# Optimization experiments

Hardware: AMD Instinct MI355X
Metric: run time of the kernel (lower is better)

Reference implementation:

```python
import jax, jax.numpy as jnp
import numpy as np

B, S, HID = 1, 2048, 2048
NH, NKV, HD = 32, 8, 64
INTER = 8192
EPS = 1e-6


def rmsnorm(x, w, eps=EPS):
    xf = x.astype(jnp.float32)
    inv = jax.lax.rsqrt(jnp.mean(xf * xf, axis=-1, keepdims=True) + eps)
    return (xf * inv * w).astype(x.dtype)


def rope(x, sin_t, cos_t):
    # x: [B, S, H, D]; sin/cos: [S, D//2]
    sin = sin_t[None, :, None, :]
    cos = cos_t[None, :, None, :]
    d2 = x.shape[-1] // 2
    x0, x1 = x[..., :d2], x[..., d2:]
    return jnp.concatenate((x0 * cos - x1 * sin, x0 * sin + x1 * cos), axis=-1)


def setup_inputs() -> dict:
    key = jax.random.key(0)
    ks = jax.random.split(key, 12)
    hidden_states = jax.random.normal(ks[0], (B, S, HID), dtype=jnp.float32)
    # realistic RoPE tables
    inv_freq = 1.0 / (10000.0 ** (np.arange(0, HD // 2, dtype=np.float32) * 2.0 / HD))
    ang = np.arange(S, dtype=np.float32)[:, None] * inv_freq[None, :]
    sin_table = jnp.asarray(np.sin(ang))
    cos_table = jnp.asarray(np.cos(ang))
    s = 0.02
    return {
        "hidden_states": hidden_states,
        "sin_table": sin_table,
        "cos_table": cos_table,
        "ln1_w": jnp.ones((HID,), jnp.float32),
        "ln2_w": jnp.ones((HID,), jnp.float32),
        "wq": jax.random.normal(ks[1], (HID, NH * HD), jnp.float32) * s,
        "wk": jax.random.normal(ks[2], (HID, NKV * HD), jnp.float32) * s,
        "wv": jax.random.normal(ks[3], (HID, NKV * HD), jnp.float32) * s,
        "wo": jax.random.normal(ks[4], (NH * HD, HID), jnp.float32) * s,
        "w_gate": jax.random.normal(ks[5], (HID, INTER), jnp.float32) * s,
        "w_up": jax.random.normal(ks[6], (HID, INTER), jnp.float32) * s,
        "w_down": jax.random.normal(ks[7], (INTER, HID), jnp.float32) * s,
    }


def attention(x, sin_t, cos_t, wq, wk, wv, wo):
    b, s, _ = x.shape
    q = (x @ wq).reshape(b, s, NH, HD)
    k = (x @ wk).reshape(b, s, NKV, HD)
    v = (x @ wv).reshape(b, s, NKV, HD).transpose(0, 2, 1, 3)  # [B,Hk,S,D]
    q = rope(q, sin_t, cos_t).transpose(0, 2, 1, 3)  # [B,Hq,S,D]
    k = rope(k, sin_t, cos_t).transpose(0, 2, 1, 3)  # [B,Hk,S,D]
    g = NH // NKV
    k = jnp.repeat(k, g, axis=1)
    v = jnp.repeat(v, g, axis=1)
    scale = 1.0 / np.sqrt(HD)
    scores = jnp.einsum("bhqd,bhkd->bhqk", q, k) * scale
    mask = jnp.tril(jnp.ones((s, s), dtype=bool))
    scores = jnp.where(mask, scores, -jnp.inf)
    probs = jax.nn.softmax(scores, axis=-1)
    out = jnp.einsum("bhqk,bhkd->bhqd", probs, v)
    out = out.transpose(0, 2, 1, 3).reshape(b, s, NH * HD)
    return out @ wo


def reference(hidden_states, sin_table, cos_table, ln1_w, ln2_w, wq, wk, wv, wo, w_gate, w_up, w_down):
    x = hidden_states
    x = x + attention(rmsnorm(x, ln1_w), sin_table, cos_table, wq, wk, wv, wo)
    h = rmsnorm(x, ln2_w)
    x = x + (jax.nn.silu(h @ w_gate) * (h @ w_up)) @ w_down
    return x
```

## Files before the change

kernel.cpp:

```cpp
#include <hip/hip_runtime.h>
#include <hip/hip_bf16.h>

typedef float f32x4 __attribute__((ext_vector_type(4)));
typedef unsigned int u32x4 __attribute__((ext_vector_type(4)));
typedef unsigned int u32x2 __attribute__((ext_vector_type(2)));
typedef _Float16 f16x4 __attribute__((ext_vector_type(4)));
typedef unsigned short u16;

#define S_LEN 2048
#define HID 2048
#define NHEAD 32
#define NKVH 8
#define HDIM 64

__device__ __forceinline__ unsigned short f2bf_bits(float f) {
    unsigned int u = __builtin_bit_cast(unsigned int, f);
    unsigned int r = u + 0x7fffu + ((u >> 16) & 1u);
    return (unsigned short)(r >> 16);
}
__device__ __forceinline__ float bf2f(unsigned short b) {
    unsigned int u = ((unsigned int)b) << 16;
    return __builtin_bit_cast(float, u);
}
__device__ __forceinline__ unsigned cvt_pk_bf16(float lo, float hi) {
    unsigned d;
    asm("v_cvt_pk_bf16_f32 %0, %1, %2" : "=v"(d) : "v"(lo), "v"(hi));
    return d;
}

__device__ __forceinline__ f32x4 mfma_bf16(u32x4 a, u32x4 b, f32x4 c) {
    asm("v_mfma_f32_16x16x32_bf16 %0, %1, %2, %0" : "+v"(c) : "v"(a), "v"(b));
    return c;
}

__device__ __forceinline__ void gload_lds16(const void* g, void* l) {
    __builtin_amdgcn_global_load_lds(
        (const __attribute__((address_space(1))) void*)g,
        (__attribute__((address_space(3))) void*)l, 16, 0, 0);
}

__global__ __launch_bounds__(256)
void rmsnorm_k(const float* __restrict__ x, const float* __restrict__ wgt,
               unsigned short* __restrict__ out)
{
    int row = blockIdx.x;
    int t = threadIdx.x;
    const float* xr = x + (size_t)row * HID;
    f32x4 a = *(const f32x4*)(xr + t * 8);
    f32x4 b = *(const f32x4*)(xr + t * 8 + 4);
    float s = 0.f;
#pragma unroll
    for (int i = 0; i < 4; ++i) s += a[i] * a[i] + b[i] * b[i];
#pragma unroll
    for (int off = 32; off > 0; off >>= 1) s += __shfl_down(s, off);
    __shared__ float red[4];
    if ((t & 63) == 0) red[t >> 6] = s;
    __syncthreads();
    float tot = red[0] + red[1] + red[2] + red[3];
    float inv = rsqrtf(tot * (1.0f / (float)HID) + 1e-6f);
    f32x4 wa = *(const f32x4*)(wgt + t * 8);
    f32x4 wb = *(const f32x4*)(wgt + t * 8 + 4);
    unsigned int pk[4];
#pragma unroll
    for (int i = 0; i < 2; ++i) {
        pk[i]     = (unsigned)f2bf_bits(a[2*i] * inv * wa[2*i]) |
                    ((unsigned)f2bf_bits(a[2*i+1] * inv * wa[2*i+1]) << 16);
        pk[i + 2] = (unsigned)f2bf_bits(b[2*i] * inv * wb[2*i]) |
                    ((unsigned)f2bf_bits(b[2*i+1] * inv * wb[2*i+1]) << 16);
    }
    u32x4 ov; ov[0] = pk[0]; ov[1] = pk[1]; ov[2] = pk[2]; ov[3] = pk[3];
    *(u32x4*)(out + (size_t)row * HID + t * 8) = ov;
}

__global__ __launch_bounds__(256)
void transpose_cvt(const float* __restrict__ in, unsigned short* __restrict__ out,
                   int K, int N)
{
    __shared__ unsigned short tile[64 * 65];
    int kb = blockIdx.y * 64, nb = blockIdx.x * 64;
    int t = threadIdx.x;
    int r = t >> 2, c0 = (t & 3) * 16;
    const float* src = in + (size_t)(kb + r) * N + nb + c0;
#pragma unroll
    for (int j = 0; j < 4; ++j) {
        f32x4 v = *(const f32x4*)(src + j * 4);
#pragma unroll
        for (int i = 0; i < 4; ++i)
            tile[r * 65 + c0 + j * 4 + i] = f2bf_bits(v[i]);
    }
    __syncthreads();
    unsigned short e[16];
#pragma unroll
    for (int j = 0; j < 16; ++j) e[j] = tile[(c0 + j) * 65 + r];
    u32x4 o0, o1;
#pragma unroll
    for (int j = 0; j < 4; ++j) {
        o0[j] = (unsigned)e[2*j] | ((unsigned)e[2*j+1] << 16);
        o1[j] = (unsigned)e[8 + 2*j] | ((unsigned)e[8 + 2*j+1] << 16);
    }
    unsigned short* dst = out + (size_t)(nb + r) * K + kb + c0;
    *(u32x4*)(dst) = o0;
    *(u32x4*)(dst + 8) = o1;
}

__global__ __launch_bounds__(256)
void rope_k(unsigned short* __restrict__ qkv, const float* __restrict__ sin_t,
            const float* __restrict__ cos_t)
{
    int s = blockIdx.x;
    for (int it = threadIdx.x; it < (NHEAD + NKVH) * 32; it += 256) {
        int slot = it >> 5;
        int d = it & 31;
        int col = (slot < NHEAD) ? slot * 64 + d : HID + (slot - NHEAD) * 64 + d;
        unsigned short* p = qkv + (size_t)s * 3072 + col;
        float x0 = bf2f(p[0]);
        float x1 = bf2f(p[32]);
        float c = cos_t[s * 32 + d];
        float sn = sin_t[s * 32 + d];
        p[0]  = f2bf_bits(x0 * c - x1 * sn);
        p[32] = f2bf_bits(x0 * sn + x1 * c);
    }
}

__global__ __launch_bounds__(256)
void transpose_v(const unsigned short* __restrict__ qkv, unsigned short* __restrict__ vT)
{
    __shared__ unsigned short tile[64][80];
    int kb = blockIdx.x * 64, kvh = blockIdx.y;
    int t = threadIdx.x;
    int r = t >> 2, c0 = (t & 3) * 16;
    const unsigned short* src = qkv + (size_t)(kb + r) * 3072 + 2560 + kvh * 64 + c0;
    u32x4 v0 = *(const u32x4*)(src);
    u32x4 v1 = *(const u32x4*)(src + 8);
    *(u32x4*)&tile[r][c0] = v0;
    *(u32x4*)&tile[r][c0 + 8] = v1;
    __syncthreads();
    int d = t >> 2, k0 = (t & 3) * 16;
    unsigned short e[16];
#pragma unroll
    for (int j = 0; j < 16; ++j) e[j] = tile[k0 + j][d];
    u32x4 o0, o1;
#pragma unroll
    for (int j = 0; j < 4; ++j) {
        o0[j] = (unsigned)e[2*j] | ((unsigned)e[2*j+1] << 16);
        o1[j] = (unsigned)e[8 + 2*j] | ((unsigned)e[8 + 2*j+1] << 16);
    }
    int s0 = ((k0 >> 3) ^ (d & 7)) & 7;
    int s1 = (((k0 >> 3) + 1) ^ (d & 7)) & 7;
    unsigned short* dst = vT + ((size_t)kvh * 64 + d) * 2048 + kb;
    *(u32x4*)(dst + s0 * 8) = o0;
    *(u32x4*)(dst + s1 * 8) = o1;
}

template <int EPI>
__global__ __launch_bounds__(256)
void gemm_bt(const unsigned short* __restrict__ A,
             const unsigned short* __restrict__ Bt,
             void* __restrict__ outp, const void* __restrict__ auxp,
             int M, int N, int Kc, int lda)
{
    __shared__ unsigned short As[2][128 * 32];
    __shared__ unsigned short Bs[2][128 * 32];
    int t = threadIdx.x, w = t >> 6, l = t & 63;
    int rb = blockIdx.y, cb = blockIdx.x, zb = blockIdx.z;
    int wr = w >> 1, wc = w & 1;
    int l4 = l >> 4, l15 = l & 15;
    int arow = l >> 2, acol = (l & 3) * 8;
    f32x4 acc[4][4] = {};
    const unsigned short* Ag = A + (size_t)rb * 128 * lda + (size_t)zb * Kc
                                 + (size_t)(w * 16 + arow) * lda + acol;
    const unsigned short* Bg = Bt + (size_t)cb * 128 * lda + (size_t)zb * Kc
                                 + (size_t)(w * 16 + arow) * lda + acol;
    int nk = Kc >> 5;

#define STAGE(buf, kt)                                                          \
    {                                                                           \
        const unsigned short* Agk = Ag + (size_t)(kt) * 32;                     \
        const unsigned short* Bgk = Bg + (size_t)(kt) * 32;                     \
        gload_lds16(Agk, &As[buf][w * 512]);                                    \
        gload_lds16(Agk + (size_t)64 * lda, &As[buf][(4 + w) * 512]);           \
        gload_lds16(Bgk, &Bs[buf][w * 512]);                                    \
        gload_lds16(Bgk + (size_t)64 * lda, &Bs[buf][(4 + w) * 512]);           \
    }

    STAGE(0, 0);
    __syncthreads();
    int cur = 0;
    for (int kt = 0; kt < nk; ++kt) {
        if (kt + 1 < nk) STAGE(cur ^ 1, kt + 1);
        u32x4 af[4], bfr[4];
#pragma unroll
        for (int i = 0; i < 4; ++i)
            af[i] = *(const u32x4*)(&As[cur][(wr * 64 + i * 16 + l15) * 32 + l4 * 8]);
#pragma unroll
        for (int n = 0; n < 4; ++n)
            bfr[n] = *(const u32x4*)(&Bs[cur][(wc * 64 + n * 16 + l15) * 32 + l4 * 8]);
#pragma unroll
        for (int i = 0; i < 4; ++i)
#pragma unroll
            for (int n = 0; n < 4; ++n)
                acc[i][n] = mfma_bf16(af[i], bfr[n], acc[i][n]);
        __syncthreads();
        cur ^= 1;
    }
#undef STAGE

    int row0 = rb * 128 + wr * 64 + l4 * 4;
    int col0 = cb * 128 + wc * 64 + l15;
#pragma unroll
    for (int i = 0; i < 4; ++i) {
#pragma unroll
        for (int n = 0; n < 4; ++n) {
#pragma unroll
            for (int r = 0; r < 4; ++r) {
                int row = row0 + i * 16 + r;
                int col = col0 + n * 16;
                size_t idx = (size_t)row * N + col;
                float v = acc[i][n][r];
                if (EPI == 0) {
                    ((unsigned short*)outp)[idx] = f2bf_bits(v);
                } else if (EPI == 3) {
                    ((float*)outp)[idx] = v + ((const float*)auxp)[idx];
                } else {
                    ((_Float16*)outp)[(size_t)zb * M * N + idx] = (_Float16)v;
                }
            }
        }
    }
}

template <int KK, int QUAD>
__device__ __forceinline__ void phase8(u16* lds, int cur, f32x4 (&acc)[8][4],
                                       u32x4 (&bfv)[4],
                                       int aoff, int boff,
                                       const u16* Asrc, const u16* Bsrc,
                                       int lda, int kt_stage,
                                       int dst0, int dst1)
{
    const u16* ah = lds + (cur * 4 + KK * 2) * 8192 + aoff + QUAD * 2048;
    u32x4 af[4];
#pragma unroll
    for (int mi = 0; mi < 4; ++mi) af[mi] = *(const u32x4*)(ah + mi * 512);
    if (QUAD == 0) {
        const u16* bh = lds + (cur * 4 + KK * 2 + 1) * 8192 + boff;
#pragma unroll
        for (int ni = 0; ni < 4; ++ni) bfv[ni] = *(const u32x4*)(bh + ni * 512);
    }
    {
        const u16* src = (QUAD ? Bsrc : Asrc) + (size_t)kt_stage * 64 + (KK == 0 ? 32 : 0);
        int dbuf = (KK == 0) ? (cur ^ 1) : cur;
        int slot = (KK == 0) ? (2 + QUAD) : QUAD;
        u16* d = lds + (dbuf * 4 + slot) * 8192;
        gload_lds16(src, d + dst0);
        gload_lds16(src + (size_t)128 * lda, d + dst1);
    }
    __builtin_amdgcn_s_barrier();
    asm volatile("s_waitcnt lgkmcnt(0)" ::: "memory");
    __builtin_amdgcn_sched_barrier(0);
    __builtin_amdgcn_s_setprio(1);
#pragma unroll
    for (int mi = 0; mi < 4; ++mi)
#pragma unroll
        for (int ni = 0; ni < 4; ++ni)
            acc[QUAD * 4 + mi][ni] = mfma_bf16(af[mi], bfv[ni], acc[QUAD * 4 + mi][ni]);
    __builtin_amdgcn_s_setprio(0);
    if (QUAD == 1) asm volatile("s_waitcnt vmcnt(8)" ::: "memory");
    __builtin_amdgcn_s_barrier();
}

template <int EPI>
__global__ __launch_bounds__(512, 2)
void gemm8p(const u16* __restrict__ A, const u16* __restrict__ Bt,
            void* __restrict__ outp, const void* __restrict__ auxp,
            int M, int N, int Kc, int lda)
{
    extern __shared__ u16 lds[];
    const int tid = threadIdx.x;
    const int w = tid >> 6, l = tid & 63;
    const int wm = w >> 2, wn = w & 3;
    const int l4 = l >> 4, l15 = l & 15;
    const int zb = blockIdx.y;

    int wg = blockIdx.x, nwg = gridDim.x;
    int swzb = ((nwg & 7) == 0) ? ((wg & 7) * (nwg >> 3) + (wg >> 3)) : wg;
    int rbs = M >> 8;
    int rb = swzb % rbs, cb = swzb / rbs;

    const int sw = ((tid & 3) ^ ((tid >> 3) & 3)) * 8;
    const int srow = tid >> 2;
    const u16* Asrc = A + (size_t)(rb * 256 + srow) * lda + (size_t)zb * Kc + sw;
    const u16* Bsrc = Bt + (size_t)(cb * 256 + srow) * lda + (size_t)zb * Kc + sw;
    const int dst0 = tid * 8, dst1 = (512 + tid) * 8;

    const int rswz = (l15 >> 1) & 3;
    const int aoff = (wm * 128 + l15) * 32 + (l4 ^ rswz) * 8;
    const int boff = (wn * 64 + l15) * 32 + (l4 ^ rswz) * 8;

    f32x4 acc[8][4] = {};
    u32x4 bfv[4];
    const int NT = Kc >> 6;

    {
#pragma unroll
        for (int h = 0; h < 2; ++h) {
            const u16* sA = Asrc + h * 32;
            const u16* sB = Bsrc + h * 32;
            gload_lds16(sA, lds + (h * 2) * 8192 + dst0);
            gload_lds16(sA + (size_t)128 * lda, lds + (h * 2) * 8192 + dst1);
            gload_lds16(sB, lds + (h * 2 + 1) * 8192 + dst0);
            gload_lds16(sB + (size_t)128 * lda, lds + (h * 2 + 1) * 8192 + dst1);
        }
        int t1 = (NT > 1) ? 1 : 0;
        const u16* sA = Asrc + (size_t)t1 * 64;
        const u16* sB = Bsrc + (size_t)t1 * 64;
        gload_lds16(sA, lds + (4 + 0) * 8192 + dst0);
        gload_lds16(sA + (size_t)128 * lda, lds + (4 + 0) * 8192 + dst1);
        gload_lds16(sB, lds + (4 + 1) * 8192 + dst0);
        gload_lds16(sB + (size_t)128 * lda, lds + (4 + 1) * 8192 + dst1);
    }
    asm volatile("s_waitcnt vmcnt(8)" ::: "memory");
    __builtin_amdgcn_s_barrier();

    for (int t = 0; t < NT; ++t) {
        int cur = t & 1;
        int k1 = (t + 1 < NT) ? t + 1 : 0;
        int k2 = (t + 2 < NT) ? t + 2 : 0;
        phase8<0, 0>(lds, cur, acc, bfv, aoff, boff, Asrc, Bsrc, lda, k1, dst0, dst1);
        phase8<0, 1>(lds, cur, acc, bfv, aoff, boff, Asrc, Bsrc, lda, k1, dst0, dst1);
        phase8<1, 0>(lds, cur, acc, bfv, aoff, boff, Asrc, Bsrc, lda, k2, dst0, dst1);
        phase8<1, 1>(lds, cur, acc, bfv, aoff, boff, Asrc, Bsrc, lda, k2, dst0, dst1);
    }
    asm volatile("s_waitcnt vmcnt(0)" ::: "memory");

    int row0 = rb * 256 + wm * 128 + l4 * 4;
    int col0 = cb * 256 + wn * 64 + l15;
#pragma unroll
    for (int mi = 0; mi < 8; ++mi) {
#pragma unroll
        for (int ni = 0; ni < 4; ++ni) {
#pragma unroll
            for (int r = 0; r < 4; ++r) {
                int row = row0 + mi * 16 + r;
                int col = col0 + ni * 16;
                size_t idx = (size_t)row * N + col;
                float v = acc[mi][ni][r];
                if (EPI == 1) {
                    float sv = v / (1.0f + __expf(-v));
                    ((unsigned short*)outp)[idx] = f2bf_bits(sv);
                } else if (EPI == 2) {
                    float gv = bf2f(((const unsigned short*)auxp)[idx]);
                    ((unsigned short*)outp)[idx] = f2bf_bits(v * gv);
                } else {
                    ((_Float16*)outp)[(size_t)zb * M * N + idx] = (_Float16)v;
                }
            }
        }
    }
}

__global__ __launch_bounds__(256)
void reduce_add4(float* __restrict__ out, const _Float16* __restrict__ p, int n)
{
    int i = (blockIdx.x * 256 + threadIdx.x) * 4;
    f32x4 a = *(const f32x4*)(out + i);
#pragma unroll
    for (int z = 0; z < 4; ++z) {
        f16x4 h = *(const f16x4*)(p + (size_t)z * n + i);
#pragma unroll
        for (int j = 0; j < 4; ++j) a[j] += (float)h[j];
    }
    *(f32x4*)(out + i) = a;
}

__global__ __launch_bounds__(256)
void reduce_res2(float* __restrict__ out, const float* __restrict__ x,
                 const _Float16* __restrict__ p, int n)
{
    int i = (blockIdx.x * 256 + threadIdx.x) * 4;
    f32x4 a = *(const f32x4*)(x + i);
#pragma unroll
    for (int z = 0; z < 2; ++z) {
        f16x4 h = *(const f16x4*)(p + (size_t)z * n + i);
#pragma unroll
        for (int j = 0; j < 4; ++j) a[j] += (float)h[j];
    }
    *(f32x4*)(out + i) = a;
}

__global__ __launch_bounds__(256)
void attn_fwd(const unsigned short* __restrict__ qkv,
              const unsigned short* __restrict__ vT,
              unsigned short* __restrict__ out)
{
    int p = blockIdx.x, h = blockIdx.y, kvh = h >> 2;
    int t = threadIdx.x, w = t >> 6, l = t & 63;
    int l4 = l >> 4, l15 = l & 15;
    __shared__ unsigned short Ks[2][64 * 64];
    __shared__ unsigned short Vs[2][64 * 64];

    const unsigned short* Kg = qkv + HID + kvh * 64;
    const unsigned short* Vg = vT + (size_t)kvh * 64 * 2048;

    int ch0 = w * 2, ch1 = w * 2 + 1;
    int rsub = l >> 3;
    int ksw = ((l & 7) ^ (rsub & 7)) * 8;
    int vcol = (l & 7) * 8;
    int sw0 = (l4 ^ (l15 & 7)) * 8;
    int sw1 = ((l4 | 4) ^ (l15 & 7)) * 8;
    int srcA = ((l >> 4) & 1) * 32 + l15;
    int srcB = srcA + 16;
    bool hi32 = (l & 32) != 0;

#define STAGE_KV(buf, kt)                                                         \
    {                                                                             \
        gload_lds16(Kg + (size_t)((kt) * 64 + ch0 * 8 + rsub) * 3072 + ksw,       \
                    &Ks[buf][ch0 * 512]);                                         \
        gload_lds16(Kg + (size_t)((kt) * 64 + ch1 * 8 + rsub) * 3072 + ksw,       \
                    &Ks[buf][ch1 * 512]);                                         \
        gload_lds16(Vg + (size_t)(ch0 * 8 + rsub) * 2048 + (kt) * 64 + vcol,      \
                    &Vs[buf][ch0 * 512]);                                         \
        gload_lds16(Vg + (size_t)(ch1 * 8 + rsub) * 2048 + (kt) * 64 + vcol,      \
                    &Vs[buf][ch1 * 512]);                                         \
    }

    const float SC2 = 0.18033688f;
    const float THR = 44.36f;
    const float BIG = -3.0e38f;

    for (int half = 0; half < 2; ++half) {
        int qb = half ? (31 - p) : p;
        int qrow0 = qb * 64 + w * 16;
        STAGE_KV(0, 0);
        const unsigned short* qg = qkv + (size_t)(qrow0 + l15) * 3072 + h * 64 + l4 * 8;
        u32x4 aq0 = *(const u32x4*)(qg);
        u32x4 aq1 = *(const u32x4*)(qg + 32);
        f32x4 o[4] = {};
        float m = BIG, ls = 0.f;
        __syncthreads();
        int cur = 0;
        for (int kt = 0; kt <= qb; ++kt) {
            if (kt < qb) STAGE_KV(cur ^ 1, kt + 1);
            f32x4 sc[4];
#pragma unroll
            for (int n = 0; n < 4; ++n) {
                const unsigned short* kb_ = &Ks[cur][(n * 16 + l15) * 64];
                u32x4 b0 = *(const u32x4*)(kb_ + sw0);
                u32x4 b1 = *(const u32x4*)(kb_ + sw1);
                f32x4 z = {};
                z = mfma_bf16(b0, aq0, z);
                z = mfma_bf16(b1, aq1, z);
                sc[n] = z;
            }
            if (kt == qb) {
                int qloc = w * 16 + l15;
#pragma unroll
                for (int n = 0; n < 4; ++n)
#pragma unroll
                    for (int r = 0; r < 4; ++r)
                        if (n * 16 + l4 * 4 + r > qloc) sc[n][r] = BIG;
            }
            float rmax = BIG;
#pragma unroll
            for (int n = 0; n < 4; ++n)
#pragma unroll
                for (int r = 0; r < 4; ++r) rmax = fmaxf(rmax, sc[n][r]);
            rmax = fmaxf(rmax, __shfl_xor(rmax, 16));
            rmax = fmaxf(rmax, __shfl_xor(rmax, 32));
            if (__ballot(rmax - m > THR)) {
                float mn = fmaxf(m, rmax);
                float al = __builtin_exp2f((m - mn) * SC2);
                m = mn;
                ls *= al;
#pragma unroll
                for (int nd = 0; nd < 4; ++nd)
#pragma unroll
                    for (int r = 0; r < 4; ++r) o[nd][r] *= al;
            }
            float ms = m * SC2, rs = 0.f;
#pragma unroll
            for (int n = 0; n < 4; ++n)
#pragma unroll
                for (int r = 0; r < 4; ++r) {
                    float pe = __builtin_exp2f(__builtin_fmaf(sc[n][r], SC2, -ms));
                    sc[n][r] = pe;
                    rs += pe;
                }
            rs += __shfl_xor(rs, 16);
            rs += __shfl_xor(rs, 32);
            ls += rs;
            unsigned pk0[2], pk1[2], pk2[2], pk3[2];
#pragma unroll
            for (int rr = 0; rr < 2; ++rr) {
                pk0[rr] = cvt_pk_bf16(sc[0][2*rr], sc[0][2*rr+1]);
                pk1[rr] = cvt_pk_bf16(sc[1][2*rr], sc[1][2*rr+1]);
                pk2[rr] = cvt_pk_bf16(sc[2][2*rr], sc[2][2*rr+1]);
                pk3[rr] = cvt_pk_bf16(sc[3][2*rr], sc[3][2*rr+1]);
            }
            u32x4 W1, W2;
            {
                unsigned a0, a1;
                a0 = __shfl(pk0[0], srcA); a1 = __shfl(pk1[0], srcA); W1[0] = hi32 ? a1 : a0;
                a0 = __shfl(pk0[1], srcA); a1 = __shfl(pk1[1], srcA); W1[1] = hi32 ? a1 : a0;
                a0 = __shfl(pk0[0], srcB); a1 = __shfl(pk1[0], srcB); W1[2] = hi32 ? a1 : a0;
                a0 = __shfl(pk0[1], srcB); a1 = __shfl(pk1[1], srcB); W1[3] = hi32 ? a1 : a0;
                a0 = __shfl(pk2[0], srcA); a1 = __shfl(pk3[0], srcA); W2[0] = hi32 ? a1 : a0;
                a0 = __shfl(pk2[1], srcA); a1 = __shfl(pk3[1], srcA); W2[1] = hi32 ? a1 : a0;
                a0 = __shfl(pk2[0], srcB); a1 = __shfl(pk3[0], srcB); W2[2] = hi32 ? a1 : a0;
                a0 = __shfl(pk2[1], srcB); a1 = __shfl(pk3[1], srcB); W2[3] = hi32 ? a1 : a0;
            }
#pragma unroll
            for (int nd = 0; nd < 4; ++nd) {
                const unsigned short* vb = &Vs[cur][(nd * 16 + l15) * 64];
                u32x4 bv0 = *(const u32x4*)(vb + sw0);
                u32x4 bv1 = *(const u32x4*)(vb + sw1);
                o[nd] = mfma_bf16(bv0, W1, o[nd]);
                o[nd] = mfma_bf16(bv1, W2, o[nd]);
            }
            __syncthreads();
            cur ^= 1;
        }
#undef STAGE_KV
        float linv = 1.0f / ls;
        unsigned short* orow = out + (size_t)(qrow0 + l15) * HID + h * 64 + l4 * 4;
#pragma unroll
        for (int nd = 0; nd < 4; ++nd) {
            u32x2 wv;
            wv[0] = cvt_pk_bf16(o[nd][0] * linv, o[nd][1] * linv);
            wv[1] = cvt_pk_bf16(o[nd][2] * linv, o[nd][3] * linv);
            *(u32x2*)(orow + nd * 16) = wv;
        }
    }
}

extern "C" void kernel_launch(void* const* d_in, const int* in_sizes, int n_in,
                              void* d_out, int out_size, void* d_ws, size_t ws_size,
                              hipStream_t stream)
{
    const float* x     = (const float*)d_in[0];
    const float* sin_t = (const float*)d_in[1];
    const float* cos_t = (const float*)d_in[2];
    const float* ln1w  = (const float*)d_in[3];
    const float* ln2w  = (const float*)d_in[4];
    const float* wq    = (const float*)d_in[5];
    const float* wk    = (const float*)d_in[6];
    const float* wv    = (const float*)d_in[7];
    const float* wo    = (const float*)d_in[8];
    const float* wg    = (const float*)d_in[9];
    const float* wu    = (const float*)d_in[10];
    const float* wd    = (const float*)d_in[11];
    float* out = (float*)d_out;

    char* ws = (char*)d_ws;
    if (ws_size < 113246208u) return;
    unsigned short* wT   = (unsigned short*)(ws);
    unsigned short* xn   = (unsigned short*)(ws + 33554432u);
    unsigned short* qkv  = (unsigned short*)(ws + 41943040u);
    unsigned short* attn = (unsigned short*)(ws + 54525952u);
    unsigned short* vT   = (unsigned short*)(ws + 62914560u);
    _Float16*       part = (_Float16*)(ws + 33554432u);
    unsigned short* g    = (unsigned short*)(ws + 79691776u);
    _Float16*       opart = (_Float16*)(ws + 79691776u);

    hipFuncSetAttribute(reinterpret_cast<const void*>(&gemm8p<1>),
                        hipFuncAttributeMaxDynamicSharedMemorySize, 131072);
    hipFuncSetAttribute(reinterpret_cast<const void*>(&gemm8p<2>),
                        hipFuncAttributeMaxDynamicSharedMemorySize, 131072);
    hipFuncSetAttribute(reinterpret_cast<const void*>(&gemm8p<5>),
                        hipFuncAttributeMaxDynamicSharedMemorySize, 131072);

    rmsnorm_k<<<S_LEN, 256, 0, stream>>>(x, ln1w, xn);

    transpose_cvt<<<dim3(32, 32), 256, 0, stream>>>(wq, wT, 2048, 2048);
    transpose_cvt<<<dim3(8, 32), 256, 0, stream>>>(wk, wT + (size_t)2048 * 2048, 2048, 512);
    transpose_cvt<<<dim3(8, 32), 256, 0, stream>>>(wv, wT + (size_t)2560 * 2048, 2048, 512);

    gemm_bt<0><<<dim3(24, 16, 1), 256, 0, stream>>>(xn, wT, qkv, nullptr, 2048, 3072, 2048, 2048);

    rope_k<<<S_LEN, 256, 0, stream>>>(qkv, sin_t, cos_t);
    transpose_v<<<dim3(32, 8), 256, 0, stream>>>(qkv, vT);

    attn_fwd<<<dim3(16, 32), 256, 0, stream>>>(qkv, vT, attn);

    transpose_cvt<<<dim3(32, 32), 256, 0, stream>>>(wo, wT, 2048, 2048);
    gemm_bt<5><<<dim3(16, 16, 2), 256, 0, stream>>>(attn, wT, opart, nullptr, 2048, 2048, 1024, 2048);
    reduce_res2<<<4096, 256, 0, stream>>>(out, x, opart, 4194304);

    rmsnorm_k<<<S_LEN, 256, 0, stream>>>(out, ln2w, xn);

    transpose_cvt<<<dim3(128, 32), 256, 0, stream>>>(wg, wT, 2048, 8192);
    gemm8p<1><<<dim3(256, 1), 512, 131072, stream>>>(xn, wT, g, nullptr, 2048, 8192, 2048, 2048);

    transpose_cvt<<<dim3(128, 32), 256, 0, stream>>>(wu, wT, 2048, 8192);
    gemm8p<2><<<dim3(256, 1), 512, 131072, stream>>>(xn, wT, g, g, 2048, 8192, 2048, 2048);

    transpose_cvt<<<dim3(32, 128), 256, 0, stream>>>(wd, wT, 8192, 2048);
    gemm8p<5><<<dim3(64, 4), 512, 131072, stream>>>(g, wT, part, nullptr, 2048, 2048, 2048, 8192);

    reduce_add4<<<4096, 256, 0, stream>>>(out, part, 4194304);
}
```

Before: 450.0 us.

## Fuse gate and up projections into one GEMM with SiLU-multiply epilogue

Adds a gemm8p_gu kernel that loads both the gate and up weight tiles for the same 128-column block and computes both accumulators in one pass. It applies silu(gate)*up in the epilogue and writes bf16 once, instead of writing g and re-reading it in a second GEMM. This removes one full read of the activations and a 32 MB intermediate round trip. The output projection also moves from gemm_bt with split-K 2 to gemm8p with split-K 4, and the residual reduce now sums four partials. The cost is a larger per-block working set, 32 accumulator tiles per wave, and a workspace layout reshuffled so the wu transpose lands where qkv/attn previously lived.

```diff
diff --git a/kernel.cpp b/kernel.cpp
--- a/kernel.cpp
+++ b/kernel.cpp
@@ -358,6 +358,134 @@
     }
 }
 
+template <int KK, int QUAD>
+__device__ __forceinline__ void phase8gu(u16* lds, int cur, f32x4 (&acc)[8][4],
+                                         u32x4 (&bfv)[4],
+                                         int aoff, int boffg, int boffu,
+                                         const u16* Asrc, const u16* Bg, const u16* Bu,
+                                         int lda, int kt_stage,
+                                         int dst0, int dst1)
+{
+    const u16* ah = lds + (cur * 4 + KK * 2) * 8192 + aoff + QUAD * 2048;
+    u32x4 af[4];
+#pragma unroll
+    for (int mi = 0; mi < 4; ++mi) af[mi] = *(const u32x4*)(ah + mi * 512);
+    if (QUAD == 0) {
+        const u16* bh = lds + (cur * 4 + KK * 2 + 1) * 8192;
+#pragma unroll
+        for (int ni = 0; ni < 2; ++ni) {
+            bfv[ni]     = *(const u32x4*)(bh + boffg + ni * 512);
+            bfv[ni + 2] = *(const u32x4*)(bh + boffu + ni * 512);
+        }
+    }
+    {
+        int koff = (size_t)0 + (KK == 0 ? 32 : 0);
+        int dbuf = (KK == 0) ? (cur ^ 1) : cur;
+        int slot = (KK == 0) ? (2 + QUAD) : QUAD;
+        u16* d = lds + (dbuf * 4 + slot) * 8192;
+        if (QUAD == 0) {
+            const u16* src = Asrc + (size_t)kt_stage * 64 + koff;
+            gload_lds16(src, d + dst0);
+            gload_lds16(src + (size_t)128 * lda, d + dst1);
+        } else {
+            gload_lds16(Bg + (size_t)kt_stage * 64 + koff, d + dst0);
+            gload_lds16(Bu + (size_t)kt_stage * 64 + koff, d + dst1);
+        }
+    }
+    __builtin_amdgcn_s_barrier();
+    asm volatile("s_waitcnt lgkmcnt(0)" ::: "memory");
+    __builtin_amdgcn_sched_barrier(0);
+    __builtin_amdgcn_s_setprio(1);
+#pragma unroll
+    for (int mi = 0; mi < 4; ++mi)
+#pragma unroll
+        for (int ni = 0; ni < 4; ++ni)
+            acc[QUAD * 4 + mi][ni] = mfma_bf16(af[mi], bfv[ni], acc[QUAD * 4 + mi][ni]);
+    __builtin_amdgcn_s_setprio(0);
+    if (QUAD == 1) asm volatile("s_waitcnt vmcnt(8)" ::: "memory");
+    __builtin_amdgcn_s_barrier();
+}
+
+__global__ __launch_bounds__(512, 2)
+void gemm8p_gu(const u16* __restrict__ A, const u16* __restrict__ WgT,
+               const u16* __restrict__ WuT, unsigned short* __restrict__ outp,
+               int M, int Nfull, int K)
+{
+    extern __shared__ u16 lds[];
+    const int tid = threadIdx.x;
+    const int w = tid >> 6, l = tid & 63;
+    const int wm = w >> 2, wn = w & 3;
+    const int l4 = l >> 4, l15 = l & 15;
+
+    int wg = blockIdx.x, nwg = gridDim.x;
+    int swzb = ((nwg & 7) == 0) ? ((wg & 7) * (nwg >> 3) + (wg >> 3)) : wg;
+    int rbs = M >> 8;
+    int rb = swzb % rbs, cb = swzb / rbs;
+
+    const int sw = ((tid & 3) ^ ((tid >> 3) & 3)) * 8;
+    const int srow = tid >> 2;
+    const u16* Asrc = A + (size_t)(rb * 256 + srow) * K + sw;
+    const u16* Bg = WgT + (size_t)(cb * 128 + srow) * K + sw;
+    const u16* Bu = WuT + (size_t)(cb * 128 + srow) * K + sw;
+    const int dst0 = tid * 8, dst1 = (512 + tid) * 8;
+
+    const int rswz = (l15 >> 1) & 3;
+    const int aoff  = (wm * 128 + l15) * 32 + (l4 ^ rswz) * 8;
+    const int boffg = (wn * 32 + l15) * 32 + (l4 ^ rswz) * 8;
+    const int boffu = (128 + wn * 32 + l15) * 32 + (l4 ^ rswz) * 8;
+
+    f32x4 acc[8][4] = {};
+    u32x4 bfv[4];
+    const int NT = K >> 6;
+
+    {
+#pragma unroll
+        for (int h = 0; h < 2; ++h) {
+            const u16* sA = Asrc + h * 32;
+            gload_lds16(sA, lds + (h * 2) * 8192 + dst0);
+            gload_lds16(sA + (size_t)128 * K, lds + (h * 2) * 8192 + dst1);
+            gload_lds16(Bg + h * 32, lds + (h * 2 + 1) * 8192 + dst0);
+            gload_lds16(Bu + h * 32, lds + (h * 2 + 1) * 8192 + dst1);
+        }
+        const u16* sA = Asrc + 64;
+        gload_lds16(sA, lds + (4 + 0) * 8192 + dst0);
+        gload_lds16(sA + (size_t)128 * K, lds + (4 + 0) * 8192 + dst1);
+        gload_lds16(Bg + 64, lds + (4 + 1) * 8192 + dst0);
+        gload_lds16(Bu + 64, lds + (4 + 1) * 8192 + dst1);
+    }
+    asm volatile("s_waitcnt vmcnt(8)" ::: "memory");
+    __builtin_amdgcn_s_barrier();
+
+    for (int t = 0; t < NT; ++t) {
+        int cur = t & 1;
+        int k1 = (t + 1 < NT) ? t + 1 : 0;
+        int k2 = (t + 2 < NT) ? t + 2 : 0;
+        phase8gu<0, 0>(lds, cur, acc, bfv, aoff, boffg, boffu, Asrc, Bg, Bu, K, k1, dst0, dst1);
+        phase8gu<0, 1>(lds, cur, acc, bfv, aoff, boffg, boffu, Asrc, Bg, Bu, K, k1, dst0, dst1);
+        phase8gu<1, 0>(lds, cur, acc, bfv, aoff, boffg, boffu, Asrc, Bg, Bu, K, k2, dst0, dst1);
+        phase8gu<1, 1>(lds, cur, acc, bfv, aoff, boffg, boffu, Asrc, Bg, Bu, K, k2, dst0, dst1);
+    }
+    asm volatile("s_waitcnt vmcnt(0)" ::: "memory");
+
+    int row0 = rb * 256 + wm * 128 + l4 * 4;
+    int col0 = cb * 128 + wn * 32 + l15;
+#pragma unroll
+    for (int mi = 0; mi < 8; ++mi) {
+#pragma unroll
+        for (int ni = 0; ni < 2; ++ni) {
+#pragma unroll
+            for (int r = 0; r < 4; ++r) {
+                int row = row0 + mi * 16 + r;
+                int col = col0 + ni * 16;
+                float gv = acc[mi][ni][r];
+                float uv = acc[mi][ni + 2][r];
+                float sv = gv / (1.0f + __expf(-gv)) * uv;
+                outp[(size_t)row * Nfull + col] = f2bf_bits(sv);
+            }
+        }
+    }
+}
+
 __global__ __launch_bounds__(256)
 void reduce_add4(float* __restrict__ out, const _Float16* __restrict__ p, int n)
 {
@@ -373,13 +501,13 @@
 }
 
 __global__ __launch_bounds__(256)
-void reduce_res2(float* __restrict__ out, const float* __restrict__ x,
+void reduce_res4(float* __restrict__ out, const float* __restrict__ x,
                  const _Float16* __restrict__ p, int n)
 {
     int i = (blockIdx.x * 256 + threadIdx.x) * 4;
     f32x4 a = *(const f32x4*)(x + i);
 #pragma unroll
-    for (int z = 0; z < 2; ++z) {
+    for (int z = 0; z < 4; ++z) {
         f16x4 h = *(const f16x4*)(p + (size_t)z * n + i);
 #pragma unroll
         for (int j = 0; j < 4; ++j) a[j] += (float)h[j];
@@ -552,20 +680,19 @@
 
     char* ws = (char*)d_ws;
     if (ws_size < 113246208u) return;
-    unsigned short* wT   = (unsigned short*)(ws);
-    unsigned short* xn   = (unsigned short*)(ws + 33554432u);
-    unsigned short* qkv  = (unsigned short*)(ws + 41943040u);
-    unsigned short* attn = (unsigned short*)(ws + 54525952u);
-    unsigned short* vT   = (unsigned short*)(ws + 62914560u);
-    _Float16*       part = (_Float16*)(ws + 33554432u);
-    unsigned short* g    = (unsigned short*)(ws + 79691776u);
+    unsigned short* wT    = (unsigned short*)(ws);
+    unsigned short* xn    = (unsigned short*)(ws + 33554432u);
+    unsigned short* qkv   = (unsigned short*)(ws + 41943040u);
+    unsigned short* attn  = (unsigned short*)(ws + 54525952u);
+    unsigned short* vT    = (unsigned short*)(ws + 62914560u);
+    unsigned short* wuT   = (unsigned short*)(ws + 41943040u);
+    _Float16*       part  = (_Float16*)(ws + 41943040u);
+    unsigned short* g     = (unsigned short*)(ws + 79691776u);
     _Float16*       opart = (_Float16*)(ws + 79691776u);
 
-    hipFuncSetAttribute(reinterpret_cast<const void*>(&gemm8p<1>),
+    hipFuncSetAttribute(reinterpret_cast<const void*>(&gemm8p<5>),
                         hipFuncAttributeMaxDynamicSharedMemorySize, 131072);
-    hipFuncSetAttribute(reinterpret_cast<const void*>(&gemm8p<2>),
-                        hipFuncAttributeMaxDynamicSharedMemorySize, 131072);
-    hipFuncSetAttribute(reinterpret_cast<const void*>(&gemm8p<5>),
+    hipFuncSetAttribute(reinterpret_cast<const void*>(&gemm8p_gu),
                         hipFuncAttributeMaxDynamicSharedMemorySize, 131072);
 
     rmsnorm_k<<<S_LEN, 256, 0, stream>>>(x, ln1w, xn);
@@ -582,16 +709,14 @@
     attn_fwd<<<dim3(16, 32), 256, 0, stream>>>(qkv, vT, attn);
 
     transpose_cvt<<<dim3(32, 32), 256, 0, stream>>>(wo, wT, 2048, 2048);
-    gemm_bt<5><<<dim3(16, 16, 2), 256, 0, stream>>>(attn, wT, opart, nullptr, 2048, 2048, 1024, 2048);
-    reduce_res2<<<4096, 256, 0, stream>>>(out, x, opart, 4194304);
+    gemm8p<5><<<dim3(64, 4), 512, 131072, stream>>>(attn, wT, opart, nullptr, 2048, 2048, 512, 2048);
+    reduce_res4<<<4096, 256, 0, stream>>>(out, x, opart, 4194304);
 
     rmsnorm_k<<<S_LEN, 256, 0, stream>>>(out, ln2w, xn);
 
     transpose_cvt<<<dim3(128, 32), 256, 0, stream>>>(wg, wT, 2048, 8192);
-    gemm8p<1><<<dim3(256, 1), 512, 131072, stream>>>(xn, wT, g, nullptr, 2048, 8192, 2048, 2048);
-
-    transpose_cvt<<<dim3(128, 32), 256, 0, stream>>>(wu, wT, 2048, 8192);
-    gemm8p<2><<<dim3(256, 1), 512, 131072, stream>>>(xn, wT, g, g, 2048, 8192, 2048, 2048);
+    transpose_cvt<<<dim3(128, 32), 256, 0, stream>>>(wu, wuT, 2048, 8192);
+    gemm8p_gu<<<dim3(512), 512, 131072, stream>>>(xn, wT, wuT, g, 2048, 8192, 2048);
 
     transpose_cvt<<<dim3(32, 128), 256, 0, stream>>>(wd, wT, 8192, 2048);
     gemm8p<5><<<dim3(64, 4), 512, 131072, stream>>>(g, wT, part, nullptr, 2048, 2048, 2048, 8192);
```

After: 434.0 us. 1.04x faster.
